# Performance work log

Measured on AMD Instinct MI355X. Metric: run time of the kernel, lower is better.

The kernel has to match this reference:

```python
import jax, jax.numpy as jnp
import numpy as np


def _block_diag(blocks):
    """blocks: [K, m, n] -> dense block-diagonal [K*m, K*n] (vectorized scatter)."""
    K, m, n = blocks.shape
    out = jnp.zeros((K * m, K * n), blocks.dtype)
    r = jnp.arange(K)[:, None, None] * m + jnp.arange(m)[None, :, None]
    c = jnp.arange(K)[:, None, None] * n + jnp.arange(n)[None, None, :]
    return out.at[r, c].set(blocks)


def setup_inputs() -> dict:
    key = jax.random.key(0)
    k0, k1, k2, k3, k4 = jax.random.split(key, 5)
    n_state, n_input, T = 32, 16, 64
    n_all = n_state + n_input
    A = jax.random.normal(k0, (n_state, n_state), jnp.float32) * 0.3
    B = jax.random.normal(k1, (n_state, n_input), jnp.float32)
    M = jax.random.normal(k2, (T, n_all, n_all), jnp.float32)
    # symmetric PSD per-step cost blocks so the KKT matrix is invertible
    C = jnp.einsum('tij,tkj->tik', M, M) / n_all + 0.1 * jnp.eye(n_all, dtype=jnp.float32)
    c = jax.random.normal(k3, (T, n_all), jnp.float32)
    x0 = jax.random.normal(k4, (n_state,), jnp.float32)
    return {"A": A, "B": B, "C": C, "c": c, "T": T, "x0": x0}


def reference(A, B, C, c, T, x0):
    n_state = A.shape[0]
    n_input = B.shape[1]
    n_all = n_state + n_input

    # cost_mat = block_diag(C_0, ..., C_{T-1})  -> [n_all*T, n_all*T]
    cost_mat = _block_diag(C)

    # dynamics constraint matrix [n_state*T, n_all*T]
    AB = jnp.concatenate((A, B), axis=1)  # [n_state, n_all]
    AB_bd = _block_diag(jnp.broadcast_to(AB, (T - 1, n_state, n_all)) + jnp.zeros((T - 1, 1, 1), A.dtype))
    dynamics = jnp.zeros((n_state * T, n_all * T), A.dtype)
    dynamics = dynamics.at[:n_state, :n_state].set(jnp.eye(n_state, dtype=A.dtype))
    dynamics = dynamics.at[n_state:n_state * T, :n_all * (T - 1)].set(AB_bd)
    # -I coupling: rows n_state*t + i, cols n_all*t + i for t = 1..T-1
    rows = n_state * jnp.arange(1, T)[:, None] + jnp.arange(n_state)[None, :]
    cols = n_all * jnp.arange(1, T)[:, None] + jnp.arange(n_state)[None, :]
    dynamics = dynamics.at[rows, cols].set(-1.0)

    zero_mat = jnp.zeros((n_state * T, n_state * T), A.dtype)
    full_mat = jnp.block([[cost_mat, dynamics.T], [dynamics, zero_mat]])

    sol = jnp.zeros(n_all * T + n_state * T, A.dtype)
    sol = sol.at[n_all * T:n_all * T + n_state].set(x0)

    tau_mu = jnp.linalg.solve(full_mat, sol[:, None])[:, 0]
    tau_star = tau_mu[:n_all * T]
    mu_star = tau_mu[n_all * T:]
    return (tau_star, mu_star)
```

## Files before the change

kernel.cpp:

```cpp
#include <hip/hip_runtime.h>

#define NS 32
#define NI 16
#define NA 48
#define TT 64
#define HT 32
#define CSZ (NA * NA)
#define C4  (CSZ / 4)

__device__ __forceinline__ double fast_rcp(double x) {
    double r = (double)(1.0f / (float)x);
    r = r * (2.0 - x * r);
    r = r * (2.0 - x * r);
    return r;
}

__launch_bounds__(256, 1)
__global__ void lqr_fast(const float* __restrict__ Ag,
                         const float* __restrict__ Bg,
                         const float* __restrict__ Cg,
                         const float* __restrict__ x0g,
                         float* __restrict__ out,
                         float* __restrict__ Kall,
                         float* __restrict__ Pall)
{
    __shared__ float4 sC4[2][C4];
    __shared__ float  sXT[TT][NS];
    __shared__ double sA[NS][33];
    __shared__ double sB[NS][17];
    __shared__ double sP[NS][33];
    __shared__ double sPA[NS][33];
    __shared__ double sPB[NS][17];
    __shared__ double sHs[NI][33];
    __shared__ double sKt[NI][33];
    __shared__ double sGi[NI][17];
    __shared__ double sPp[NS][33];

    const int tid  = threadIdx.x;
    const int wid  = tid >> 6, lane = tid & 63;
    const int pi   = tid >> 3, pj0 = (tid & 7) * 4, pb0 = (tid & 7) * 2;
    const int ki   = tid >> 4, kj0 = (tid & 15) * 2;

    for (int idx = tid; idx < NS * NS; idx += 256) {
        sA[idx >> 5][idx & 31] = (double)Ag[idx];
        sP[idx >> 5][idx & 31] = 0.0;
    }
    for (int idx = tid; idx < NS * NI; idx += 256) sB[idx >> 4][idx & 15] = (double)Bg[idx];
    {
        const float4* src = (const float4*)(Cg + (TT - 1) * CSZ);
        sC4[0][tid]       = src[tid];
        sC4[0][tid + 256] = src[tid + 256];
        if (tid < C4 - 512) sC4[0][tid + 512] = src[tid + 512];
    }
    __syncthreads();

    int cur = 0;
    for (int t = TT - 1; t >= 0; --t) {
        const float* sCf = (const float*)sC4[cur];

        {
            double a0 = 0, a1 = 0, a2 = 0, a3 = 0, b0 = 0, b1 = 0;
            for (int k = 0; k < NS; ++k) {
                const double p = sP[pi][k];
                a0 += p * sA[k][pj0 + 0]; a1 += p * sA[k][pj0 + 1];
                a2 += p * sA[k][pj0 + 2]; a3 += p * sA[k][pj0 + 3];
                b0 += p * sB[k][pb0 + 0]; b1 += p * sB[k][pb0 + 1];
            }
            sPA[pi][pj0 + 0] = a0; sPA[pi][pj0 + 1] = a1;
            sPA[pi][pj0 + 2] = a2; sPA[pi][pj0 + 3] = a3;
            sPB[pi][pb0 + 0] = b0; sPB[pi][pb0 + 1] = b1;
        }
        __syncthreads();

        float4 pf0 = {}, pf1 = {}, pf2 = {};
        const bool doPf = (t > 0);
        if (doPf) {
            const float4* src = (const float4*)(Cg + (t - 1) * CSZ);
            pf0 = src[tid];
            pf1 = src[tid + 256];
            if (tid >= 64 && tid < 128) pf2 = src[tid + 448];
        }

        if (wid == 0) {
            const int ri = lane & 15, cg = lane >> 4, jb = cg * 4;
            const float4 rv = *(const float4*)&sCf[(NS + ri) * NA + NS + jb];
            double g0 = (double)rv.x, g1 = (double)rv.y;
            double g2 = (double)rv.z, g3 = (double)rv.w;
            for (int k = 0; k < NS; ++k) {
                const double b = sB[k][ri];
                g0 += b * sPB[k][jb + 0]; g1 += b * sPB[k][jb + 1];
                g2 += b * sPB[k][jb + 2]; g3 += b * sPB[k][jb + 3];
            }
#pragma unroll
            for (int k = 0; k < NI; ++k) {
                const double myslot = ((k & 3) == 0) ? g0 : ((k & 3) == 1) ? g1
                                     : ((k & 3) == 2) ? g2 : g3;
                const int    plv  = k + ((k >> 2) << 4);
                const double piv  = __shfl(myslot, plv, 64);
                const double cv   = __shfl(myslot, ri + ((k >> 2) << 4), 64);
                const double pr0  = __shfl(g0, k + (cg << 4), 64);
                const double pr1  = __shfl(g1, k + (cg << 4), 64);
                const double pr2  = __shfl(g2, k + (cg << 4), 64);
                const double pr3  = __shfl(g3, k + (cg << 4), 64);
                const double ip   = fast_rcp(piv);
                const bool   rk   = (ri == k);
                g0 = rk ? ((jb + 0 == k) ? ip : pr0 * ip)
                        : ((jb + 0 == k) ? -cv * ip : g0 - cv * pr0 * ip);
                g1 = rk ? ((jb + 1 == k) ? ip : pr1 * ip)
                        : ((jb + 1 == k) ? -cv * ip : g1 - cv * pr1 * ip);
                g2 = rk ? ((jb + 2 == k) ? ip : pr2 * ip)
                        : ((jb + 2 == k) ? -cv * ip : g2 - cv * pr2 * ip);
                g3 = rk ? ((jb + 3 == k) ? ip : pr3 * ip)
                        : ((jb + 3 == k) ? -cv * ip : g3 - cv * pr3 * ip);
            }
            sGi[ri][jb + 0] = g0; sGi[ri][jb + 1] = g1;
            sGi[ri][jb + 2] = g2; sGi[ri][jb + 3] = g3;
        } else {
            const int e0 = tid - 64;
            for (int e = e0; e < NI * NS; e += 192) {
                const int i = e >> 5, j = e & 31;
                double acc = (double)sCf[j * NA + NS + i];
                for (int k = 0; k < NS; ++k) acc += sB[k][i] * sPA[k][j];
                sHs[i][j] = acc;
            }
            for (int e = e0; e < NS * NS; e += 192) {
                const int i = e >> 5, j = e & 31;
                double acc = (double)sCf[i * NA + j];
                for (int k = 0; k < NS; ++k) acc += sA[k][i] * sPA[k][j];
                sPp[i][j] = acc;
            }
        }

        if (doPf) {
            float4* dst = sC4[cur ^ 1];
            dst[tid]       = pf0;
            dst[tid + 256] = pf1;
            if (tid >= 64 && tid < 128) dst[tid + 448] = pf2;
        }
        __syncthreads();

        {
            double a0 = 0, a1 = 0;
            for (int k = 0; k < NI; ++k) {
                const double g = sGi[ki][k];
                a0 += g * sHs[k][kj0 + 0];
                a1 += g * sHs[k][kj0 + 1];
            }
            sKt[ki][kj0 + 0] = a0; sKt[ki][kj0 + 1] = a1;
            Kall[t * NI * NS + ki * NS + kj0 + 0] = (float)a0;
            Kall[t * NI * NS + ki * NS + kj0 + 1] = (float)a1;
        }
        __syncthreads();

        {
            double a0 = sPp[pi][pj0 + 0], a1 = sPp[pi][pj0 + 1];
            double a2 = sPp[pi][pj0 + 2], a3 = sPp[pi][pj0 + 3];
            for (int k = 0; k < NI; ++k) {
                const double h = sHs[k][pi];
                a0 -= h * sKt[k][pj0 + 0]; a1 -= h * sKt[k][pj0 + 1];
                a2 -= h * sKt[k][pj0 + 2]; a3 -= h * sKt[k][pj0 + 3];
            }
            double b0 = sPp[pj0 + 0][pi], b1 = sPp[pj0 + 1][pi];
            double b2 = sPp[pj0 + 2][pi], b3 = sPp[pj0 + 3][pi];
            for (int k = 0; k < NI; ++k) {
                const double hk = sKt[k][pi];
                b0 -= sHs[k][pj0 + 0] * hk; b1 -= sHs[k][pj0 + 1] * hk;
                b2 -= sHs[k][pj0 + 2] * hk; b3 -= sHs[k][pj0 + 3] * hk;
            }
            const double r0 = 0.5 * (a0 + b0), r1 = 0.5 * (a1 + b1);
            const double r2 = 0.5 * (a2 + b2), r3 = 0.5 * (a3 + b3);
            sP[pi][pj0 + 0] = r0; sP[pi][pj0 + 1] = r1;
            sP[pi][pj0 + 2] = r2; sP[pi][pj0 + 3] = r3;
            float* Pt = Pall + t * NS * NS + pi * NS + pj0;
            Pt[0] = (float)r0; Pt[1] = (float)r1; Pt[2] = (float)r2; Pt[3] = (float)r3;
        }
        __syncthreads();
        cur ^= 1;
    }

    if (wid == 0) {
        const int row = lane & 31;
        double x = 0.0;
        if (lane < NS) x = (double)x0g[lane];
        for (int t = 0; t < TT; ++t) {
            if (lane < NS) {
                const float xv = (float)x;
                sXT[t][lane] = xv;
                out[t * NA + lane] = xv;
            }
            const float* Kt = Kall + t * NI * NS + (lane & 15) * NS;
            double accU = 0.0;
            for (int k = 0; k < NS; ++k) {
                const double xk = __shfl(x, k, 64);
                accU += (double)Kt[k] * xk;
            }
            const double u = -accU;
            if (lane < NI) out[t * NA + NS + lane] = (float)u;
            if (t < TT - 1) {
                double accX = 0.0;
                for (int k = 0; k < NS; ++k) {
                    const double xk = __shfl(x, k, 64);
                    accX += sA[row][k] * xk;
                }
                for (int k = 0; k < NI; ++k) {
                    const double uk = __shfl(u, k, 64);
                    accX += sB[row][k] * uk;
                }
                x = accX;
            }
        }
    }
    __syncthreads();

    for (int e = tid; e < TT * NS; e += 256) {
        const int t = e >> 5, i = e & 31;
        const float* Pt = Pall + t * NS * NS + i * NS;
        double acc = 0.0;
        for (int k = 0; k < NS; ++k) acc += (double)Pt[k] * (double)sXT[t][k];
        if (t == 0) acc = -acc;
        out[NA * TT + t * NS + i] = (float)acc;
    }
}

__launch_bounds__(256, 1)
__global__ void lqr_kernel_fb(const float* __restrict__ Ag,
                              const float* __restrict__ Bg,
                              const float* __restrict__ Cg,
                              const float* __restrict__ x0g,
                              float* __restrict__ out)
{
    __shared__ float  sKh[HT][NI][NS];
    __shared__ float  sXT[TT][NS];
    __shared__ double sA[NS][NS];
    __shared__ double sB[NS][NI];
    __shared__ double sP[NS][NS];
    __shared__ double sPA[NS][NS];
    __shared__ double sPB[NS][NI];
    __shared__ double sHs[NI][NS];
    __shared__ double sKt[NI][NS];
    __shared__ double sGi[NI][NI];
    __shared__ double sPp[NS][NS];
    __shared__ double sx[2][NS];
    __shared__ double su[NI];

    const int tid  = threadIdx.x;
    const int wid  = tid >> 6, lane = tid & 63;
    const int pi   = tid >> 3, pj0 = (tid & 7) * 4, pb0 = (tid & 7) * 2;
    const int ki   = tid >> 4, kj0 = (tid & 15) * 2;

    for (int idx = tid; idx < NS * NS; idx += 256) sA[idx >> 5][idx & 31] = (double)Ag[idx];
    for (int idx = tid; idx < NS * NI; idx += 256) sB[idx >> 4][idx & 15] = (double)Bg[idx];
    __syncthreads();

    auto step = [&](int t, bool storeK, int kbase, bool emitMu) {
        const float* Ct = Cg + t * NA * NA;
        {
            double a0 = 0, a1 = 0, a2 = 0, a3 = 0, b0 = 0, b1 = 0;
            for (int k = 0; k < NS; ++k) {
                const double p = sP[pi][k];
                a0 += p * sA[k][pj0 + 0]; a1 += p * sA[k][pj0 + 1];
                a2 += p * sA[k][pj0 + 2]; a3 += p * sA[k][pj0 + 3];
                b0 += p * sB[k][pb0 + 0]; b1 += p * sB[k][pb0 + 1];
            }
            sPA[pi][pj0 + 0] = a0; sPA[pi][pj0 + 1] = a1;
            sPA[pi][pj0 + 2] = a2; sPA[pi][pj0 + 3] = a3;
            sPB[pi][pb0 + 0] = b0; sPB[pi][pb0 + 1] = b1;
        }
        __syncthreads();
        if (wid == 0) {
            const int ri = lane & 15, cg = lane >> 4, jb = cg * 4;
            double g0 = (double)Ct[(NS + ri) * NA + NS + jb + 0];
            double g1 = (double)Ct[(NS + ri) * NA + NS + jb + 1];
            double g2 = (double)Ct[(NS + ri) * NA + NS + jb + 2];
            double g3 = (double)Ct[(NS + ri) * NA + NS + jb + 3];
            for (int k = 0; k < NS; ++k) {
                const double b = sB[k][ri];
                g0 += b * sPB[k][jb + 0]; g1 += b * sPB[k][jb + 1];
                g2 += b * sPB[k][jb + 2]; g3 += b * sPB[k][jb + 3];
            }
#pragma unroll
            for (int k = 0; k < NI; ++k) {
                const double myslot = ((k & 3) == 0) ? g0 : ((k & 3) == 1) ? g1
                                     : ((k & 3) == 2) ? g2 : g3;
                const int    plv  = k + ((k >> 2) << 4);
                const double piv  = __shfl(myslot, plv, 64);
                const double cv   = __shfl(myslot, ri + ((k >> 2) << 4), 64);
                const double pr0  = __shfl(g0, k + (cg << 4), 64);
                const double pr1  = __shfl(g1, k + (cg << 4), 64);
                const double pr2  = __shfl(g2, k + (cg << 4), 64);
                const double pr3  = __shfl(g3, k + (cg << 4), 64);
                const double ip   = 1.0 / piv;
                const bool   rk   = (ri == k);
                g0 = rk ? ((jb + 0 == k) ? ip : pr0 * ip)
                        : ((jb + 0 == k) ? -cv * ip : g0 - cv * pr0 * ip);
                g1 = rk ? ((jb + 1 == k) ? ip : pr1 * ip)
                        : ((jb + 1 == k) ? -cv * ip : g1 - cv * pr1 * ip);
                g2 = rk ? ((jb + 2 == k) ? ip : pr2 * ip)
                        : ((jb + 2 == k) ? -cv * ip : g2 - cv * pr2 * ip);
                g3 = rk ? ((jb + 3 == k) ? ip : pr3 * ip)
                        : ((jb + 3 == k) ? -cv * ip : g3 - cv * pr3 * ip);
            }
            sGi[ri][jb + 0] = g0; sGi[ri][jb + 1] = g1;
            sGi[ri][jb + 2] = g2; sGi[ri][jb + 3] = g3;
        } else {
            const int e0 = tid - 64;
            for (int e = e0; e < NI * NS; e += 192) {
                const int i = e >> 5, j = e & 31;
                double acc = (double)Ct[j * NA + NS + i];
                for (int k = 0; k < NS; ++k) acc += sB[k][i] * sPA[k][j];
                sHs[i][j] = acc;
            }
            for (int e = e0; e < NS * NS; e += 192) {
                const int i = e >> 5, j = e & 31;
                double acc = (double)Ct[i * NA + j];
                for (int k = 0; k < NS; ++k) acc += sA[k][i] * sPA[k][j];
                sPp[i][j] = acc;
            }
        }
        __syncthreads();
        {
            double a0 = 0, a1 = 0;
            for (int k = 0; k < NI; ++k) {
                const double g = sGi[ki][k];
                a0 += g * sHs[k][kj0 + 0];
                a1 += g * sHs[k][kj0 + 1];
            }
            sKt[ki][kj0 + 0] = a0; sKt[ki][kj0 + 1] = a1;
            if (storeK) {
                sKh[t - kbase][ki][kj0 + 0] = (float)a0;
                sKh[t - kbase][ki][kj0 + 1] = (float)a1;
            }
        }
        __syncthreads();
        {
            double a0 = sPp[pi][pj0 + 0], a1 = sPp[pi][pj0 + 1];
            double a2 = sPp[pi][pj0 + 2], a3 = sPp[pi][pj0 + 3];
            for (int k = 0; k < NI; ++k) {
                const double h = sHs[k][pi];
                a0 -= h * sKt[k][pj0 + 0]; a1 -= h * sKt[k][pj0 + 1];
                a2 -= h * sKt[k][pj0 + 2]; a3 -= h * sKt[k][pj0 + 3];
            }
            double b0 = sPp[pj0 + 0][pi], b1 = sPp[pj0 + 1][pi];
            double b2 = sPp[pj0 + 2][pi], b3 = sPp[pj0 + 3][pi];
            for (int k = 0; k < NI; ++k) {
                const double hk = sKt[k][pi];
                b0 -= sHs[k][pj0 + 0] * hk; b1 -= sHs[k][pj0 + 1] * hk;
                b2 -= sHs[k][pj0 + 2] * hk; b3 -= sHs[k][pj0 + 3] * hk;
            }
            sP[pi][pj0 + 0] = 0.5 * (a0 + b0); sP[pi][pj0 + 1] = 0.5 * (a1 + b1);
            sP[pi][pj0 + 2] = 0.5 * (a2 + b2); sP[pi][pj0 + 3] = 0.5 * (a3 + b3);
        }
        __syncthreads();
        if (emitMu && tid < NS) {
            double acc = 0.0;
            for (int k = 0; k < NS; ++k) acc += sP[tid][k] * (double)sXT[t][k];
            if (t == 0) acc = -acc;
            out[NA * TT + t * NS + tid] = (float)acc;
        }
    };

    auto sweep = [&](int tlo, int klo, int khi, bool emitMu) {
        for (int idx = tid; idx < NS * NS; idx += 256) sP[idx >> 5][idx & 31] = 0.0;
        __syncthreads();
        for (int t = TT - 1; t >= tlo; --t)
            step(t, (t >= klo && t < khi), klo, emitMu);
    };

    int cur = 0;
    auto forward = [&](int t0, int t1, int kbase) {
        for (int t = t0; t < t1; ++t) {
            if (tid < NS) {
                const float xv = (float)sx[cur][tid];
                sXT[t][tid] = xv;
                out[t * NA + tid] = xv;
            } else if (tid >= 64 && tid < 64 + NI) {
                const int i = tid - 64;
                double acc = 0.0;
                for (int k = 0; k < NS; ++k)
                    acc += (double)sKh[t - kbase][i][k] * sx[cur][k];
                su[i] = -acc;
                out[t * NA + NS + i] = (float)(-acc);
            }
            __syncthreads();
            if (t < TT - 1) {
                if (tid < NS) {
                    double acc = 0.0;
                    for (int k = 0; k < NS; ++k) acc += sA[tid][k] * sx[cur][k];
                    for (int k = 0; k < NI; ++k) acc += sB[tid][k] * su[k];
                    sx[cur ^ 1][tid] = acc;
                }
                __syncthreads();
                cur ^= 1;
            }
        }
    };

    sweep(0, 0, HT, false);
    if (tid < NS) sx[0][tid] = (double)x0g[tid];
    __syncthreads();
    forward(0, HT, 0);
    sweep(HT, HT, TT, false);
    forward(HT, TT, HT);
    sweep(0, 0, 0, true);
}

extern "C" void kernel_launch(void* const* d_in, const int* in_sizes, int n_in,
                              void* d_out, int out_size, void* d_ws, size_t ws_size,
                              hipStream_t stream) {
    const float *A = nullptr, *B = nullptr, *C = nullptr, *x0 = nullptr;
    for (int i = 0; i < n_in; ++i) {
        switch (in_sizes[i]) {
            case 1024:   A  = (const float*)d_in[i]; break;
            case 512:    B  = (const float*)d_in[i]; break;
            case 147456: C  = (const float*)d_in[i]; break;
            case 32:     x0 = (const float*)d_in[i]; break;
            default: break;
        }
    }
    if (!A || !B || !C || !x0) {
        A  = (const float*)d_in[0];
        B  = (const float*)d_in[1];
        C  = (const float*)d_in[2];
        x0 = (const float*)d_in[5];
    }

    const size_t need = (size_t)(TT * NI * NS + TT * NS * NS) * sizeof(float);
    if (d_ws != nullptr && ws_size >= need) {
        float* Kall = (float*)d_ws;
        float* Pall = Kall + TT * NI * NS;
        lqr_fast<<<1, 256, 0, stream>>>(A, B, C, x0, (float*)d_out, Kall, Pall);
    } else {
        lqr_kernel_fb<<<1, 256, 0, stream>>>(A, B, C, x0, (float*)d_out);
    }
}
```

Before: 614.4 us.

## Widen LQR backward sweep to 1024 threads and drop shared-memory C prefetch

Launches the single-block Riccati kernel with 1024 threads so each thread computes one element of the PA, PB, K and P updates instead of several. It also removes the double-buffered shared-memory prefetch of each step's cost block and reads C directly from global memory inside the sequential loop. More threads shorten the per-step arithmetic, but global C loads now sit on the serial critical path, and barriers across 16 waves cost more.

```diff
diff --git a/kernel.cpp b/kernel.cpp
--- a/kernel.cpp
+++ b/kernel.cpp
@@ -6,7 +6,6 @@
 #define TT 64
 #define HT 32
 #define CSZ (NA * NA)
-#define C4  (CSZ / 4)
 
 __device__ __forceinline__ double fast_rcp(double x) {
     double r = (double)(1.0f / (float)x);
@@ -15,7 +14,7 @@
     return r;
 }
 
-__launch_bounds__(256, 1)
+__launch_bounds__(1024, 1)
 __global__ void lqr_fast(const float* __restrict__ Ag,
                          const float* __restrict__ Bg,
                          const float* __restrict__ Cg,
@@ -24,7 +23,6 @@
                          float* __restrict__ Kall,
                          float* __restrict__ Pall)
 {
-    __shared__ float4 sC4[2][C4];
     __shared__ float  sXT[TT][NS];
     __shared__ double sA[NS][33];
     __shared__ double sB[NS][17];
@@ -38,54 +36,38 @@
 
     const int tid  = threadIdx.x;
     const int wid  = tid >> 6, lane = tid & 63;
-    const int pi   = tid >> 3, pj0 = (tid & 7) * 4, pb0 = (tid & 7) * 2;
-    const int ki   = tid >> 4, kj0 = (tid & 15) * 2;
-
-    for (int idx = tid; idx < NS * NS; idx += 256) {
+    const int ei   = tid >> 5, ej = tid & 31;
+
+    for (int idx = tid; idx < NS * NS; idx += 1024) {
         sA[idx >> 5][idx & 31] = (double)Ag[idx];
         sP[idx >> 5][idx & 31] = 0.0;
     }
-    for (int idx = tid; idx < NS * NI; idx += 256) sB[idx >> 4][idx & 15] = (double)Bg[idx];
-    {
-        const float4* src = (const float4*)(Cg + (TT - 1) * CSZ);
-        sC4[0][tid]       = src[tid];
-        sC4[0][tid + 256] = src[tid + 256];
-        if (tid < C4 - 512) sC4[0][tid + 512] = src[tid + 512];
-    }
+    for (int idx = tid; idx < NS * NI; idx += 1024)
+        sB[idx >> 4][idx & 15] = (double)Bg[idx];
     __syncthreads();
 
-    int cur = 0;
     for (int t = TT - 1; t >= 0; --t) {
-        const float* sCf = (const float*)sC4[cur];
-
-        {
-            double a0 = 0, a1 = 0, a2 = 0, a3 = 0, b0 = 0, b1 = 0;
-            for (int k = 0; k < NS; ++k) {
-                const double p = sP[pi][k];
-                a0 += p * sA[k][pj0 + 0]; a1 += p * sA[k][pj0 + 1];
-                a2 += p * sA[k][pj0 + 2]; a3 += p * sA[k][pj0 + 3];
-                b0 += p * sB[k][pb0 + 0]; b1 += p * sB[k][pb0 + 1];
-            }
-            sPA[pi][pj0 + 0] = a0; sPA[pi][pj0 + 1] = a1;
-            sPA[pi][pj0 + 2] = a2; sPA[pi][pj0 + 3] = a3;
-            sPB[pi][pb0 + 0] = b0; sPB[pi][pb0 + 1] = b1;
-        }
-        __syncthreads();
-
-        float4 pf0 = {}, pf1 = {}, pf2 = {};
-        const bool doPf = (t > 0);
-        if (doPf) {
-            const float4* src = (const float4*)(Cg + (t - 1) * CSZ);
-            pf0 = src[tid];
-            pf1 = src[tid + 256];
-            if (tid >= 64 && tid < 128) pf2 = src[tid + 448];
-        }
+        const float* Ct = Cg + t * CSZ;
+
+        {
+            double a = 0.0;
+            for (int k = 0; k < NS; ++k) a += sP[ei][k] * sA[k][ej];
+            sPA[ei][ej] = a;
+            if (tid < 512) {
+                const int bi = tid >> 4, bj = tid & 15;
+                double b = 0.0;
+                for (int k = 0; k < NS; ++k) b += sP[bi][k] * sB[k][bj];
+                sPB[bi][bj] = b;
+            }
+        }
+        __syncthreads();
 
         if (wid == 0) {
             const int ri = lane & 15, cg = lane >> 4, jb = cg * 4;
-            const float4 rv = *(const float4*)&sCf[(NS + ri) * NA + NS + jb];
-            double g0 = (double)rv.x, g1 = (double)rv.y;
-            double g2 = (double)rv.z, g3 = (double)rv.w;
+            double g0 = (double)Ct[(NS + ri) * NA + NS + jb + 0];
+            double g1 = (double)Ct[(NS + ri) * NA + NS + jb + 1];
+            double g2 = (double)Ct[(NS + ri) * NA + NS + jb + 2];
+            double g3 = (double)Ct[(NS + ri) * NA + NS + jb + 3];
             for (int k = 0; k < NS; ++k) {
                 const double b = sB[k][ri];
                 g0 += b * sPB[k][jb + 0]; g1 += b * sPB[k][jb + 1];
@@ -117,65 +99,41 @@
             sGi[ri][jb + 2] = g2; sGi[ri][jb + 3] = g3;
         } else {
             const int e0 = tid - 64;
-            for (int e = e0; e < NI * NS; e += 192) {
+            for (int e = e0; e < NI * NS; e += 960) {
                 const int i = e >> 5, j = e & 31;
-                double acc = (double)sCf[j * NA + NS + i];
+                double acc = (double)Ct[j * NA + NS + i];
                 for (int k = 0; k < NS; ++k) acc += sB[k][i] * sPA[k][j];
                 sHs[i][j] = acc;
             }
-            for (int e = e0; e < NS * NS; e += 192) {
+            for (int e = e0; e < NS * NS; e += 960) {
                 const int i = e >> 5, j = e & 31;
-                double acc = (double)sCf[i * NA + j];
+                double acc = (double)Ct[i * NA + j];
                 for (int k = 0; k < NS; ++k) acc += sA[k][i] * sPA[k][j];
                 sPp[i][j] = acc;
             }
         }
-
-        if (doPf) {
-            float4* dst = sC4[cur ^ 1];
-            dst[tid]       = pf0;
-            dst[tid + 256] = pf1;
-            if (tid >= 64 && tid < 128) dst[tid + 448] = pf2;
-        }
-        __syncthreads();
-
-        {
-            double a0 = 0, a1 = 0;
-            for (int k = 0; k < NI; ++k) {
-                const double g = sGi[ki][k];
-                a0 += g * sHs[k][kj0 + 0];
-                a1 += g * sHs[k][kj0 + 1];
-            }
-            sKt[ki][kj0 + 0] = a0; sKt[ki][kj0 + 1] = a1;
-            Kall[t * NI * NS + ki * NS + kj0 + 0] = (float)a0;
-            Kall[t * NI * NS + ki * NS + kj0 + 1] = (float)a1;
-        }
-        __syncthreads();
-
-        {
-            double a0 = sPp[pi][pj0 + 0], a1 = sPp[pi][pj0 + 1];
-            double a2 = sPp[pi][pj0 + 2], a3 = sPp[pi][pj0 + 3];
-            for (int k = 0; k < NI; ++k) {
-                const double h = sHs[k][pi];
-                a0 -= h * sKt[k][pj0 + 0]; a1 -= h * sKt[k][pj0 + 1];
-                a2 -= h * sKt[k][pj0 + 2]; a3 -= h * sKt[k][pj0 + 3];
-            }
-            double b0 = sPp[pj0 + 0][pi], b1 = sPp[pj0 + 1][pi];
-            double b2 = sPp[pj0 + 2][pi], b3 = sPp[pj0 + 3][pi];
-            for (int k = 0; k < NI; ++k) {
-                const double hk = sKt[k][pi];
-                b0 -= sHs[k][pj0 + 0] * hk; b1 -= sHs[k][pj0 + 1] * hk;
-                b2 -= sHs[k][pj0 + 2] * hk; b3 -= sHs[k][pj0 + 3] * hk;
-            }
-            const double r0 = 0.5 * (a0 + b0), r1 = 0.5 * (a1 + b1);
-            const double r2 = 0.5 * (a2 + b2), r3 = 0.5 * (a3 + b3);
-            sP[pi][pj0 + 0] = r0; sP[pi][pj0 + 1] = r1;
-            sP[pi][pj0 + 2] = r2; sP[pi][pj0 + 3] = r3;
-            float* Pt = Pall + t * NS * NS + pi * NS + pj0;
-            Pt[0] = (float)r0; Pt[1] = (float)r1; Pt[2] = (float)r2; Pt[3] = (float)r3;
-        }
-        __syncthreads();
-        cur ^= 1;
+        __syncthreads();
+
+        if (tid < 512) {
+            const int i = tid >> 5, j = tid & 31;
+            double a = 0.0;
+            for (int k = 0; k < NI; ++k) a += sGi[i][k] * sHs[k][j];
+            sKt[i][j] = a;
+            Kall[t * NI * NS + i * NS + j] = (float)a;
+        }
+        __syncthreads();
+
+        {
+            double a = sPp[ei][ej], b = sPp[ej][ei];
+            for (int k = 0; k < NI; ++k) {
+                a -= sHs[k][ei] * sKt[k][ej];
+                b -= sHs[k][ej] * sKt[k][ei];
+            }
+            const double r = 0.5 * (a + b);
+            sP[ei][ej] = r;
+            Pall[t * NS * NS + ei * NS + ej] = (float)r;
+        }
+        __syncthreads();
     }
 
     if (wid == 0) {
@@ -212,7 +170,7 @@
     }
     __syncthreads();
 
-    for (int e = tid; e < TT * NS; e += 256) {
+    for (int e = tid; e < TT * NS; e += 1024) {
         const int t = e >> 5, i = e & 31;
         const float* Pt = Pall + t * NS * NS + i * NS;
         double acc = 0.0;
@@ -428,7 +386,7 @@
     if (d_ws != nullptr && ws_size >= need) {
         float* Kall = (float*)d_ws;
         float* Pall = Kall + TT * NI * NS;
-        lqr_fast<<<1, 256, 0, stream>>>(A, B, C, x0, (float*)d_out, Kall, Pall);
+        lqr_fast<<<1, 1024, 0, stream>>>(A, B, C, x0, (float*)d_out, Kall, Pall);
     } else {
         lqr_kernel_fb<<<1, 256, 0, stream>>>(A, B, C, x0, (float*)d_out);
     }
```

New measurement: 823.0 us. 1.34x slower.

## Read cost blocks from global directly and register-tile the Hs/Pp products

Applied to the files above, without the earlier changes.

Drops the double-buffered shared-memory prefetch of each step's cost block and reads C entries straight from global memory inside the compute phase. The Hs and Pp computations are remapped so each thread produces 4 or 8 outputs, sharing the sA/sB/sPA loads across accumulators instead of computing one element per loop pass. Several loops get unroll pragmas and the two P-update loops are merged. The aim is to cut shared-memory traffic and loop overhead on this serial recursion, but the global loads now sit on the critical path of every time step and are no longer hidden by prefetch.

```diff
diff --git a/kernel.cpp b/kernel.cpp
--- a/kernel.cpp
+++ b/kernel.cpp
@@ -6,7 +6,6 @@
 #define TT 64
 #define HT 32
 #define CSZ (NA * NA)
-#define C4  (CSZ / 4)
 
 __device__ __forceinline__ double fast_rcp(double x) {
     double r = (double)(1.0f / (float)x);
@@ -24,7 +23,6 @@
                          float* __restrict__ Kall,
                          float* __restrict__ Pall)
 {
-    __shared__ float4 sC4[2][C4];
     __shared__ float  sXT[TT][NS];
     __shared__ double sA[NS][33];
     __shared__ double sB[NS][17];
@@ -45,21 +43,16 @@
         sA[idx >> 5][idx & 31] = (double)Ag[idx];
         sP[idx >> 5][idx & 31] = 0.0;
     }
-    for (int idx = tid; idx < NS * NI; idx += 256) sB[idx >> 4][idx & 15] = (double)Bg[idx];
-    {
-        const float4* src = (const float4*)(Cg + (TT - 1) * CSZ);
-        sC4[0][tid]       = src[tid];
-        sC4[0][tid + 256] = src[tid + 256];
-        if (tid < C4 - 512) sC4[0][tid + 512] = src[tid + 512];
-    }
+    for (int idx = tid; idx < NS * NI; idx += 256)
+        sB[idx >> 4][idx & 15] = (double)Bg[idx];
     __syncthreads();
 
-    int cur = 0;
     for (int t = TT - 1; t >= 0; --t) {
-        const float* sCf = (const float*)sC4[cur];
+        const float* Ct = Cg + t * CSZ;
 
         {
             double a0 = 0, a1 = 0, a2 = 0, a3 = 0, b0 = 0, b1 = 0;
+#pragma unroll 8
             for (int k = 0; k < NS; ++k) {
                 const double p = sP[pi][k];
                 a0 += p * sA[k][pj0 + 0]; a1 += p * sA[k][pj0 + 1];
@@ -72,20 +65,13 @@
         }
         __syncthreads();
 
-        float4 pf0 = {}, pf1 = {}, pf2 = {};
-        const bool doPf = (t > 0);
-        if (doPf) {
-            const float4* src = (const float4*)(Cg + (t - 1) * CSZ);
-            pf0 = src[tid];
-            pf1 = src[tid + 256];
-            if (tid >= 64 && tid < 128) pf2 = src[tid + 448];
-        }
-
         if (wid == 0) {
             const int ri = lane & 15, cg = lane >> 4, jb = cg * 4;
-            const float4 rv = *(const float4*)&sCf[(NS + ri) * NA + NS + jb];
-            double g0 = (double)rv.x, g1 = (double)rv.y;
-            double g2 = (double)rv.z, g3 = (double)rv.w;
+            double g0 = (double)Ct[(NS + ri) * NA + NS + jb + 0];
+            double g1 = (double)Ct[(NS + ri) * NA + NS + jb + 1];
+            double g2 = (double)Ct[(NS + ri) * NA + NS + jb + 2];
+            double g3 = (double)Ct[(NS + ri) * NA + NS + jb + 3];
+#pragma unroll 8
             for (int k = 0; k < NS; ++k) {
                 const double b = sB[k][ri];
                 g0 += b * sPB[k][jb + 0]; g1 += b * sPB[k][jb + 1];
@@ -115,32 +101,61 @@
             }
             sGi[ri][jb + 0] = g0; sGi[ri][jb + 1] = g1;
             sGi[ri][jb + 2] = g2; sGi[ri][jb + 3] = g3;
+        } else if (tid < 192) {
+            const int q  = tid - 64;
+            const int i  = q >> 3;
+            const int j0 = (q & 7) * 4;
+            double h0 = (double)Ct[(j0 + 0) * NA + NS + i];
+            double h1 = (double)Ct[(j0 + 1) * NA + NS + i];
+            double h2 = (double)Ct[(j0 + 2) * NA + NS + i];
+            double h3 = (double)Ct[(j0 + 3) * NA + NS + i];
+            double p0 = (double)Ct[i * NA + j0 + 0];
+            double p1 = (double)Ct[i * NA + j0 + 1];
+            double p2 = (double)Ct[i * NA + j0 + 2];
+            double p3 = (double)Ct[i * NA + j0 + 3];
+#pragma unroll 8
+            for (int k = 0; k < NS; ++k) {
+                const double bm = sB[k][i];
+                const double am = sA[k][i];
+                const double v0 = sPA[k][j0 + 0], v1 = sPA[k][j0 + 1];
+                const double v2 = sPA[k][j0 + 2], v3 = sPA[k][j0 + 3];
+                h0 += bm * v0; h1 += bm * v1; h2 += bm * v2; h3 += bm * v3;
+                p0 += am * v0; p1 += am * v1; p2 += am * v2; p3 += am * v3;
+            }
+            sHs[i][j0 + 0] = h0; sHs[i][j0 + 1] = h1;
+            sHs[i][j0 + 2] = h2; sHs[i][j0 + 3] = h3;
+            sPp[i][j0 + 0] = p0; sPp[i][j0 + 1] = p1;
+            sPp[i][j0 + 2] = p2; sPp[i][j0 + 3] = p3;
         } else {
-            const int e0 = tid - 64;
-            for (int e = e0; e < NI * NS; e += 192) {
-                const int i = e >> 5, j = e & 31;
-                double acc = (double)sCf[j * NA + NS + i];
-                for (int k = 0; k < NS; ++k) acc += sB[k][i] * sPA[k][j];
-                sHs[i][j] = acc;
-            }
-            for (int e = e0; e < NS * NS; e += 192) {
-                const int i = e >> 5, j = e & 31;
-                double acc = (double)sCf[i * NA + j];
-                for (int k = 0; k < NS; ++k) acc += sA[k][i] * sPA[k][j];
-                sPp[i][j] = acc;
-            }
-        }
-
-        if (doPf) {
-            float4* dst = sC4[cur ^ 1];
-            dst[tid]       = pf0;
-            dst[tid + 256] = pf1;
-            if (tid >= 64 && tid < 128) dst[tid + 448] = pf2;
+            const int s  = tid - 192;
+            const int i  = 16 + (s >> 2);
+            const int j0 = (s & 3) * 8;
+            double p0 = (double)Ct[i * NA + j0 + 0];
+            double p1 = (double)Ct[i * NA + j0 + 1];
+            double p2 = (double)Ct[i * NA + j0 + 2];
+            double p3 = (double)Ct[i * NA + j0 + 3];
+            double p4 = (double)Ct[i * NA + j0 + 4];
+            double p5 = (double)Ct[i * NA + j0 + 5];
+            double p6 = (double)Ct[i * NA + j0 + 6];
+            double p7 = (double)Ct[i * NA + j0 + 7];
+#pragma unroll 8
+            for (int k = 0; k < NS; ++k) {
+                const double am = sA[k][i];
+                p0 += am * sPA[k][j0 + 0]; p1 += am * sPA[k][j0 + 1];
+                p2 += am * sPA[k][j0 + 2]; p3 += am * sPA[k][j0 + 3];
+                p4 += am * sPA[k][j0 + 4]; p5 += am * sPA[k][j0 + 5];
+                p6 += am * sPA[k][j0 + 6]; p7 += am * sPA[k][j0 + 7];
+            }
+            sPp[i][j0 + 0] = p0; sPp[i][j0 + 1] = p1;
+            sPp[i][j0 + 2] = p2; sPp[i][j0 + 3] = p3;
+            sPp[i][j0 + 4] = p4; sPp[i][j0 + 5] = p5;
+            sPp[i][j0 + 6] = p6; sPp[i][j0 + 7] = p7;
         }
         __syncthreads();
 
         {
             double a0 = 0, a1 = 0;
+#pragma unroll
             for (int k = 0; k < NI; ++k) {
                 const double g = sGi[ki][k];
                 a0 += g * sHs[k][kj0 + 0];
@@ -155,15 +170,14 @@
         {
             double a0 = sPp[pi][pj0 + 0], a1 = sPp[pi][pj0 + 1];
             double a2 = sPp[pi][pj0 + 2], a3 = sPp[pi][pj0 + 3];
-            for (int k = 0; k < NI; ++k) {
-                const double h = sHs[k][pi];
+            double b0 = sPp[pj0 + 0][pi], b1 = sPp[pj0 + 1][pi];
+            double b2 = sPp[pj0 + 2][pi], b3 = sPp[pj0 + 3][pi];
+#pragma unroll
+            for (int k = 0; k < NI; ++k) {
+                const double h  = sHs[k][pi];
+                const double hk = sKt[k][pi];
                 a0 -= h * sKt[k][pj0 + 0]; a1 -= h * sKt[k][pj0 + 1];
                 a2 -= h * sKt[k][pj0 + 2]; a3 -= h * sKt[k][pj0 + 3];
-            }
-            double b0 = sPp[pj0 + 0][pi], b1 = sPp[pj0 + 1][pi];
-            double b2 = sPp[pj0 + 2][pi], b3 = sPp[pj0 + 3][pi];
-            for (int k = 0; k < NI; ++k) {
-                const double hk = sKt[k][pi];
                 b0 -= sHs[k][pj0 + 0] * hk; b1 -= sHs[k][pj0 + 1] * hk;
                 b2 -= sHs[k][pj0 + 2] * hk; b3 -= sHs[k][pj0 + 3] * hk;
             }
@@ -175,7 +189,6 @@
             Pt[0] = (float)r0; Pt[1] = (float)r1; Pt[2] = (float)r2; Pt[3] = (float)r3;
         }
         __syncthreads();
-        cur ^= 1;
     }
 
     if (wid == 0) {
@@ -190,6 +203,7 @@
             }
             const float* Kt = Kall + t * NI * NS + (lane & 15) * NS;
             double accU = 0.0;
+#pragma unroll 8
             for (int k = 0; k < NS; ++k) {
                 const double xk = __shfl(x, k, 64);
                 accU += (double)Kt[k] * xk;
@@ -198,10 +212,12 @@
             if (lane < NI) out[t * NA + NS + lane] = (float)u;
             if (t < TT - 1) {
                 double accX = 0.0;
+#pragma unroll 8
                 for (int k = 0; k < NS; ++k) {
                     const double xk = __shfl(x, k, 64);
                     accX += sA[row][k] * xk;
                 }
+#pragma unroll 8
                 for (int k = 0; k < NI; ++k) {
                     const double uk = __shfl(u, k, 64);
                     accX += sB[row][k] * uk;
@@ -216,6 +232,7 @@
         const int t = e >> 5, i = e & 31;
         const float* Pt = Pall + t * NS * NS + i * NS;
         double acc = 0.0;
+#pragma unroll 8
         for (int k = 0; k < NS; ++k) acc += (double)Pt[k] * (double)sXT[t][k];
         if (t == 0) acc = -acc;
         out[NA * TT + t * NS + i] = (float)acc;
```

Result: slower. 637.5 us (+3.8%).
